# Kernel optimization log

Hardware: AMD Instinct MI355X
Metric: run time of the kernel (lower is better)

The kernel has to match this reference:

```python
import jax, jax.numpy as jnp
import numpy as np

B, N, I = 8, 1024, 64
E, H, D = 2, 2, 128   # edge types, heads per layer, hidden dim
O = 64                # num_outputs
IN1 = E * H * D       # layer-1 filter input dim (concat of layer-0 heads)


def setup_inputs() -> dict:
    key = jax.random.key(0)
    ks = jax.random.split(key, 20)
    s = lambda f: 1.0 / np.sqrt(f)
    inp = {
        "nodes": jax.random.normal(ks[0], (B, N, I), jnp.float32),
        "edges": jax.random.normal(ks[1], (B, N, N, E), jnp.float32) * 0.1,
        "Wemb": jax.random.normal(ks[2], (I, D), jnp.float32) * s(I),
        "bemb": jnp.zeros((D,), jnp.float32),
        # layer 0 params: filter W, att nets a1/a2 (weight + bias), state bias
        "W0":   jax.random.normal(ks[3], (E, H, D, D), jnp.float32) * s(D),
        "A1w0": jax.random.normal(ks[4], (E, H, D), jnp.float32) * s(D),
        "A1b0": jnp.zeros((E, H), jnp.float32),
        "A2w0": jax.random.normal(ks[5], (E, H, D), jnp.float32) * s(D),
        "A2b0": jnp.zeros((E, H), jnp.float32),
        "SB0":  jnp.zeros((E, H, D), jnp.float32),
        # layer 1 params (input dim = E*H*D from concat)
        "W1":   jax.random.normal(ks[6], (E, H, IN1, D), jnp.float32) * s(IN1),
        "A1w1": jax.random.normal(ks[7], (E, H, D), jnp.float32) * s(D),
        "A1b1": jnp.zeros((E, H), jnp.float32),
        "A2w1": jax.random.normal(ks[8], (E, H, D), jnp.float32) * s(D),
        "A2b1": jnp.zeros((E, H), jnp.float32),
        "SB1":  jnp.zeros((E, H, D), jnp.float32),
        "Wout": jax.random.normal(ks[9], (D, O), jnp.float32) * s(D),
        "bout": jnp.zeros((O,), jnp.float32),
    }
    return inp


def _gat_layer(state, edges_ebnn, W, a1w, a1b, a2w, a2b, sb):
    # state: (B,N,Fin); W: (E,H,Fin,D); edges_ebnn: (E,1,B,N,N)
    Wh = jnp.einsum('bni,ehid->ehbnd', state, W)                    # (E,H,B,N,D)
    s1 = jnp.einsum('ehbnd,ehd->ehbn', Wh, a1w) + a1b[:, :, None, None]
    s2 = jnp.einsum('ehbnd,ehd->ehbn', Wh, a2w) + a2b[:, :, None, None]
    att = s1[..., :, None] + s2[..., None, :]                       # a1_i + a2_j
    att = jax.nn.leaky_relu(att, 0.2) + edges_ebnn                  # edge-type bias
    att = jax.nn.softmax(att, axis=-2)                              # torch dim=1 (over i)
    msg = jnp.einsum('ehbij,ehbjd->ehbid', att, Wh)                 # bmm aggregation
    return msg + sb[:, :, None, None, :]                            # (E,H,B,N,D)


def reference(nodes, edges, Wemb, bemb,
              W0, A1w0, A1b0, A2w0, A2b0, SB0,
              W1, A1w1, A1b1, A2w1, A2b1, SB1,
              Wout, bout):
    edges_e = jnp.transpose(edges, (3, 0, 1, 2))[:, None]           # (E,1,B,N,N)
    state = jax.nn.relu(nodes @ Wemb + bemb)                        # SlimFC embedding
    # layer 0: concat heads/edgetypes along feature dim (torch order jj outer, ii inner)
    m0 = _gat_layer(state, edges_e, W0, A1w0, A1b0, A2w0, A2b0, SB0)
    state = jnp.transpose(m0, (2, 3, 0, 1, 4)).reshape(B, N, E * H * D)
    # layer 1 (last): elu then mean over all heads/edgetypes
    m1 = jax.nn.elu(_gat_layer(state, edges_e, W1, A1w1, A1b1, A2w1, A2b1, SB1))
    state = jnp.mean(m1, axis=(0, 1))                               # (B,N,D)
    return state @ Wout + bout                                      # (B,N,O)
```

## Files before the change

kernel.cpp:

```cpp
#include <hip/hip_runtime.h>
#include <hip/hip_bf16.h>
#include <math.h>

#define NB 8
#define NN 1024
#define NI 64
#define EHC 4
#define ND 128
#define NO 64
#define FIN1 512
#define BN 8192

typedef __attribute__((ext_vector_type(8))) short short8;
typedef __attribute__((ext_vector_type(4))) float f32x4;

__device__ __forceinline__ unsigned short f2bf(float f) {
    union { float f; unsigned u; } v; v.f = f;
    unsigned r = v.u + 0x7FFF + ((v.u >> 16) & 1);
    return (unsigned short)(r >> 16);
}

__global__ void prepTk(const float* __restrict__ W0, const float* __restrict__ W1,
                       const float* __restrict__ Wemb, unsigned short* __restrict__ W0T,
                       unsigned short* __restrict__ W1T, unsigned short* __restrict__ WembT) {
    int idx = blockIdx.x * 256 + threadIdx.x;
    if (idx < EHC * ND * ND) {
        int eh = idx >> 14, d = (idx >> 7) & 127, k = idx & 127;
        W0T[idx] = f2bf(W0[((size_t)(eh * ND + k)) * ND + d]);
    }
    int idx1 = idx - EHC * ND * ND;
    if (idx1 >= 0 && idx1 < EHC * ND * FIN1) {
        int eh = idx1 >> 16;
        int r = idx1 & 65535;
        int d = r >> 9, k = r & 511;
        W1T[idx1] = f2bf(W1[((size_t)(eh * FIN1 + k)) * ND + d]);
    }
    int idx2 = idx - (EHC * ND * ND + EHC * ND * FIN1);
    if (idx2 >= 0 && idx2 < ND * NI) {
        int d = idx2 >> 6, k = idx2 & 63;
        WembT[idx2] = f2bf(Wemb[k * ND + d]);
    }
}

__global__ __launch_bounds__(256, 4) void embwh0k(
    const float* __restrict__ nodes, const unsigned short* __restrict__ WembT,
    const float* __restrict__ bemb, const unsigned short* __restrict__ W0T,
    unsigned short* __restrict__ WhT, const float* __restrict__ a1w,
    const float* __restrict__ a1b, const float* __restrict__ a2w,
    const float* __restrict__ a2b, float* __restrict__ s1, float* __restrict__ s2) {
    int id = blockIdx.x;
    int g = id & 7, s_ = id >> 3;
    int eh = s_ & 3;
    int row0 = ((s_ >> 2) * 8 + g) * 32;
    int t = threadIdx.x;
    int w = t >> 6, lane = t & 63;
    int m = lane & 15, quad = lane >> 4;

    __shared__ unsigned short stateL[32 * 136];

    f32x4 accE[2][2];
#pragma unroll
    for (int mt = 0; mt < 2; ++mt)
#pragma unroll
        for (int nt = 0; nt < 2; ++nt) accE[mt][nt] = (f32x4){0.f, 0.f, 0.f, 0.f};
#pragma unroll
    for (int kt = 0; kt < 2; ++kt) {
        short8 aE[2], bE[2];
#pragma unroll
        for (int mt = 0; mt < 2; ++mt) {
            const float* np = nodes + (size_t)(row0 + mt * 16 + m) * NI + kt * 32 + quad * 8;
            f32x4 v0 = *(const f32x4*)np;
            f32x4 v1 = *(const f32x4*)(np + 4);
            union { unsigned short us[8]; short8 s8; } pk;
#pragma unroll
            for (int r = 0; r < 4; ++r) {
                pk.us[r] = f2bf(v0[r]);
                pk.us[r + 4] = f2bf(v1[r]);
            }
            aE[mt] = pk.s8;
        }
#pragma unroll
        for (int nt = 0; nt < 2; ++nt)
            bE[nt] = *(const short8*)(WembT + (w * 32 + nt * 16 + m) * NI + kt * 32 + quad * 8);
#pragma unroll
        for (int mt = 0; mt < 2; ++mt)
#pragma unroll
            for (int nt = 0; nt < 2; ++nt)
                accE[mt][nt] =
                    __builtin_amdgcn_mfma_f32_16x16x32_bf16(aE[mt], bE[nt], accE[mt][nt], 0, 0, 0);
    }
#pragma unroll
    for (int mt = 0; mt < 2; ++mt)
#pragma unroll
        for (int nt = 0; nt < 2; ++nt) {
            int d = w * 32 + nt * 16 + m;
            float bb = bemb[d];
#pragma unroll
            for (int r = 0; r < 4; ++r) {
                float v = fmaxf(accE[mt][nt][r] + bb, 0.f);
                stateL[(mt * 16 + quad * 4 + r) * 136 + d] = f2bf(v);
            }
        }
    __syncthreads();

    f32x4 acc[2][2];
#pragma unroll
    for (int mt = 0; mt < 2; ++mt)
#pragma unroll
        for (int nt = 0; nt < 2; ++nt) acc[mt][nt] = (f32x4){0.f, 0.f, 0.f, 0.f};
#pragma unroll
    for (int k0 = 0; k0 < ND; k0 += 32) {
        short8 a[2], b[2];
#pragma unroll
        for (int mt = 0; mt < 2; ++mt)
            a[mt] = *(const short8*)&stateL[(mt * 16 + m) * 136 + k0 + quad * 8];
#pragma unroll
        for (int nt = 0; nt < 2; ++nt)
            b[nt] = *(const short8*)(W0T + ((size_t)(eh * ND + w * 32 + nt * 16 + m)) * ND +
                                     k0 + quad * 8);
#pragma unroll
        for (int mt = 0; mt < 2; ++mt)
#pragma unroll
            for (int nt = 0; nt < 2; ++nt)
                acc[mt][nt] =
                    __builtin_amdgcn_mfma_f32_16x16x32_bf16(a[mt], b[nt], acc[mt][nt], 0, 0, 0);
    }

    int b_ = row0 >> 10, i0b = row0 & 1023;
    int ehb = eh * NB + b_;
#pragma unroll
    for (int mt = 0; mt < 2; ++mt)
#pragma unroll
        for (int nt = 0; nt < 2; ++nt) {
            int d = w * 32 + nt * 16 + m;
            int i = i0b + mt * 16 + quad * 4;
            union { unsigned short us[4]; unsigned long long u64; } pk;
#pragma unroll
            for (int r = 0; r < 4; ++r) pk.us[r] = f2bf(acc[mt][nt][r]);
            *(unsigned long long*)(WhT + (((size_t)ehb) * ND + d) * NN + i) = pk.u64;
        }
    float w1a = a1w[eh * ND + w * 32 + m], w1b = a1w[eh * ND + w * 32 + 16 + m];
    float w2a = a2w[eh * ND + w * 32 + m], w2b = a2w[eh * ND + w * 32 + 16 + m];
    float p1[2][4], p2[2][4];
#pragma unroll
    for (int mt = 0; mt < 2; ++mt)
#pragma unroll
        for (int r = 0; r < 4; ++r) {
            p1[mt][r] = acc[mt][0][r] * w1a + acc[mt][1][r] * w1b;
            p2[mt][r] = acc[mt][0][r] * w2a + acc[mt][1][r] * w2b;
        }
#pragma unroll
    for (int off = 8; off >= 1; off >>= 1)
#pragma unroll
        for (int mt = 0; mt < 2; ++mt)
#pragma unroll
            for (int r = 0; r < 4; ++r) {
                p1[mt][r] += __shfl_xor(p1[mt][r], off);
                p2[mt][r] += __shfl_xor(p2[mt][r], off);
            }
    __shared__ float sred[2][4][4][8];
    if (m == 0) {
#pragma unroll
        for (int mt = 0; mt < 2; ++mt)
#pragma unroll
            for (int r = 0; r < 4; ++r) {
                sred[0][w][quad][mt * 4 + r] = p1[mt][r];
                sred[1][w][quad][mt * 4 + r] = p2[mt][r];
            }
    }
    __syncthreads();
    if (t < 32) {
        int mt = t >> 4, quad2 = (t >> 2) & 3, r = t & 3;
        int c = mt * 4 + r;
        float v = sred[0][0][quad2][c] + sred[0][1][quad2][c] + sred[0][2][quad2][c] +
                  sred[0][3][quad2][c];
        s1[(size_t)ehb * NN + i0b + t] = v + a1b[eh];
    } else if (t < 64) {
        int tl = t - 32;
        int mt = tl >> 4, quad2 = (tl >> 2) & 3, r = tl & 3;
        int c = mt * 4 + r;
        float v = sred[1][0][quad2][c] + sred[1][1][quad2][c] + sred[1][2][quad2][c] +
                  sred[1][3][quad2][c];
        s2[(size_t)ehb * NN + i0b + tl] = v + a2b[eh];
    }
}

__global__ __launch_bounds__(256, 4) void whgemm1k(
    const unsigned short* __restrict__ state, const unsigned short* __restrict__ WT,
    unsigned short* __restrict__ WhT, const float* __restrict__ a1w,
    const float* __restrict__ a1b, const float* __restrict__ a2w,
    const float* __restrict__ a2b, float* __restrict__ s1, float* __restrict__ s2) {
    int id = blockIdx.x;
    int g = id & 7, s_ = id >> 3;
    int eh = s_ & 3;
    int row0 = ((s_ >> 2) * 8 + g) * 32;
    int t = threadIdx.x;
    int w = t >> 6, lane = t & 63;
    int m = lane & 15, quad = lane >> 4;

    f32x4 acc[2][2];
#pragma unroll
    for (int mt = 0; mt < 2; ++mt)
#pragma unroll
        for (int nt = 0; nt < 2; ++nt) acc[mt][nt] = (f32x4){0.f, 0.f, 0.f, 0.f};

    const unsigned short* Ab = state + (size_t)(row0 + m) * FIN1 + quad * 8;
    const unsigned short* Bb = WT + ((size_t)eh * ND + w * 32 + m) * FIN1 + quad * 8;
#pragma unroll 4
    for (int k0 = 0; k0 < FIN1; k0 += 32) {
        short8 a[2], b[2];
#pragma unroll
        for (int mt = 0; mt < 2; ++mt)
            a[mt] = *(const short8*)(Ab + (size_t)mt * 16 * FIN1 + k0);
#pragma unroll
        for (int nt = 0; nt < 2; ++nt)
            b[nt] = *(const short8*)(Bb + (size_t)nt * 16 * FIN1 + k0);
#pragma unroll
        for (int mt = 0; mt < 2; ++mt)
#pragma unroll
            for (int nt = 0; nt < 2; ++nt)
                acc[mt][nt] =
                    __builtin_amdgcn_mfma_f32_16x16x32_bf16(a[mt], b[nt], acc[mt][nt], 0, 0, 0);
    }
    int b_ = row0 >> 10, i0b = row0 & 1023;
    int ehb = eh * NB + b_;
#pragma unroll
    for (int mt = 0; mt < 2; ++mt)
#pragma unroll
        for (int nt = 0; nt < 2; ++nt) {
            int d = w * 32 + nt * 16 + m;
            int i = i0b + mt * 16 + quad * 4;
            union { unsigned short us[4]; unsigned long long u64; } pk;
#pragma unroll
            for (int r = 0; r < 4; ++r) pk.us[r] = f2bf(acc[mt][nt][r]);
            *(unsigned long long*)(WhT + (((size_t)ehb) * ND + d) * NN + i) = pk.u64;
        }
    float w1a = a1w[eh * ND + w * 32 + m], w1b = a1w[eh * ND + w * 32 + 16 + m];
    float w2a = a2w[eh * ND + w * 32 + m], w2b = a2w[eh * ND + w * 32 + 16 + m];
    float p1[2][4], p2[2][4];
#pragma unroll
    for (int mt = 0; mt < 2; ++mt)
#pragma unroll
        for (int r = 0; r < 4; ++r) {
            p1[mt][r] = acc[mt][0][r] * w1a + acc[mt][1][r] * w1b;
            p2[mt][r] = acc[mt][0][r] * w2a + acc[mt][1][r] * w2b;
        }
#pragma unroll
    for (int off = 8; off >= 1; off >>= 1)
#pragma unroll
        for (int mt = 0; mt < 2; ++mt)
#pragma unroll
            for (int r = 0; r < 4; ++r) {
                p1[mt][r] += __shfl_xor(p1[mt][r], off);
                p2[mt][r] += __shfl_xor(p2[mt][r], off);
            }
    __shared__ float sred[2][4][4][8];
    if (m == 0) {
#pragma unroll
        for (int mt = 0; mt < 2; ++mt)
#pragma unroll
            for (int r = 0; r < 4; ++r) {
                sred[0][w][quad][mt * 4 + r] = p1[mt][r];
                sred[1][w][quad][mt * 4 + r] = p2[mt][r];
            }
    }
    __syncthreads();
    if (t < 32) {
        int mt = t >> 4, quad2 = (t >> 2) & 3, r = t & 3;
        int c = mt * 4 + r;
        float v = sred[0][0][quad2][c] + sred[0][1][quad2][c] + sred[0][2][quad2][c] +
                  sred[0][3][quad2][c];
        s1[(size_t)ehb * NN + i0b + t] = v + a1b[eh];
    } else if (t < 64) {
        int tl = t - 32;
        int mt = tl >> 4, quad2 = (tl >> 2) & 3, r = tl & 3;
        int c = mt * 4 + r;
        float v = sred[1][0][quad2][c] + sred[1][1][quad2][c] + sred[1][2][quad2][c] +
                  sred[1][3][quad2][c];
        s2[(size_t)ehb * NN + i0b + tl] = v + a2b[eh];
    }
}

__global__ __launch_bounds__(256, 4) void colsumk(const float* __restrict__ edges,
                                                  const float* __restrict__ s1,
                                                  const float* __restrict__ s2,
                                                  float* __restrict__ Spart) {
    int jt = blockIdx.x, b = blockIdx.y, ic = blockIdx.z;
    int t = threadIdx.x;
    int jp = t & 31, is = t >> 5;
    int j = jt * 64 + jp * 2;
    __shared__ float s1L[4][128];
    for (int idx = t; idx < 512; idx += 256) {
        int eh = idx >> 7;
        s1L[eh][idx & 127] = s1[((size_t)eh * NB + b) * NN + ic * 128 + (idx & 127)];
    }
    __syncthreads();
    float s2v[4][2], acc4[4][2];
#pragma unroll
    for (int eh = 0; eh < 4; ++eh) {
        s2v[eh][0] = s2[((size_t)eh * NB + b) * NN + j];
        s2v[eh][1] = s2[((size_t)eh * NB + b) * NN + j + 1];
        acc4[eh][0] = 0.f;
        acc4[eh][1] = 0.f;
    }
    const float4* ep = (const float4*)edges +
                       (size_t)(b * NN + ic * 128 + is * 16) * (NN / 2) + jt * 32 + jp;
#pragma unroll 4
    for (int ii = 0; ii < 16; ++ii) {
        float4 ev = ep[(size_t)ii * (NN / 2)];
        float s1v = s1L[0][is * 16 + ii];
#pragma unroll
        for (int eh = 0; eh < 4; ++eh) {
            float sv = s1L[eh][is * 16 + ii];
            float x0 = sv + s2v[eh][0];
            x0 = fmaxf(x0, 0.2f * x0);
            acc4[eh][0] += __expf(x0 + (eh < 2 ? ev.x : ev.y));
            float x1 = sv + s2v[eh][1];
            x1 = fmaxf(x1, 0.2f * x1);
            acc4[eh][1] += __expf(x1 + (eh < 2 ? ev.z : ev.w));
        }
        (void)s1v;
    }
    __shared__ float red[8][4][64];
#pragma unroll
    for (int eh = 0; eh < 4; ++eh) {
        red[is][eh][jp * 2] = acc4[eh][0];
        red[is][eh][jp * 2 + 1] = acc4[eh][1];
    }
    __syncthreads();
    if (t < 256) {
        int eho = t >> 6, jlo = t & 63;
        float Sv = 0.f;
#pragma unroll
        for (int isx = 0; isx < 8; ++isx) Sv += red[isx][eho][jlo];
        Spart[(((size_t)ic * EHC + eho) * NB + b) * NN + jt * 64 + jlo] = Sv;
    }
}

__global__ __launch_bounds__(512, 4) void msgk(const float* __restrict__ edges,
                                               const unsigned short* __restrict__ WhT,
                                               const float* __restrict__ s1,
                                               const float* __restrict__ s2,
                                               const float* __restrict__ Spart,
                                               const float* __restrict__ sb,
                                               unsigned short* __restrict__ out0,
                                               float* __restrict__ out1, int mode) {
    int id = blockIdx.x;
    int b = id & 7;
    int s_ = id >> 3;
    int eh = s_ & 3;
    int itile = s_ >> 2;
    int e = eh >> 1;
    int i0 = itile * 64;
    int t = threadIdx.x;
    int w = t >> 6, lane = t & 63;
    int n = lane & 15, quad = lane >> 4;
    int jl = t & 63, ib = w;

    __shared__ float2 stL[NN];
    __shared__ unsigned short pA[2][64 * 72];

    int base = (eh * NB + b) * NN;
    const size_t pstr = (size_t)EHC * NB * NN;
    for (int jj = t; jj < NN; jj += 512) {
        float S = 0.f;
#pragma unroll
        for (int ic = 0; ic < 8; ++ic) S += Spart[(size_t)ic * pstr + base + jj];
        stL[jj] = make_float2(s2[base + jj], __logf(S));
    }
    float s1r[8];
    {
        const f32x4* sp = (const f32x4*)(s1 + base + i0 + ib * 8);
        f32x4 v0 = sp[0], v1 = sp[1];
#pragma unroll
        for (int r = 0; r < 4; ++r) { s1r[r] = v0[r]; s1r[r + 4] = v1[r]; }
    }

    f32x4 acc[4];
#pragma unroll
    for (int nt = 0; nt < 4; ++nt) acc[nt] = (f32x4){0.f, 0.f, 0.f, 0.f};

    const unsigned short* Ab =
        WhT + ((size_t)base * ND + (size_t)(w * 16 + n) * NN) + quad * 8;
    const float2* ep = (const float2*)edges + (size_t)(b * NN + i0 + ib * 8) * NN + jl;
    __syncthreads();

    float2 evA[8], evB[8];
    short8 aA[2], aB[2];

    auto loadE = [&](float2* ev, int j0) {
#pragma unroll
        for (int q = 0; q < 8; ++q) ev[q] = ep[(size_t)q * NN + j0];
    };
    auto loadA = [&](short8* av, int j0) {
#pragma unroll
        for (int kt = 0; kt < 2; ++kt)
            av[kt] = *(const short8*)(Ab + kt * 32 + j0);
    };
    auto pstep = [&](const float2* ev, const short8* av, int j0, int buf) {
        float2 stj = stL[j0 + jl];
#pragma unroll
        for (int q = 0; q < 8; ++q) {
            float edge = e ? ev[q].y : ev[q].x;
            float x = s1r[q] + stj.x;
            x = fmaxf(x, 0.2f * x);
            pA[buf][(ib * 8 + q) * 72 + jl] = f2bf(__expf(x + edge - stj.y));
        }
        __syncthreads();
#pragma unroll
        for (int kt = 0; kt < 2; ++kt) {
            short8 bv[4];
#pragma unroll
            for (int nt = 0; nt < 4; ++nt)
                bv[nt] = *(const short8*)&pA[buf][(nt * 16 + n) * 72 + kt * 32 + quad * 8];
#pragma unroll
            for (int nt = 0; nt < 4; ++nt)
                acc[nt] =
                    __builtin_amdgcn_mfma_f32_16x16x32_bf16(av[kt], bv[nt], acc[nt], 0, 0, 0);
        }
    };

    loadE(evA, 0);
    loadA(aA, 0);
    for (int sp2 = 0; sp2 < 8; ++sp2) {
        int j0 = sp2 * 128;
        loadE(evB, j0 + 64);
        loadA(aB, j0 + 64);
        pstep(evA, aA, j0, 0);
        if (sp2 < 7) {
            loadE(evA, j0 + 128);
            loadA(aA, j0 + 128);
        }
        pstep(evB, aB, j0 + 64, 1);
    }

    {
        int d0 = w * 16 + quad * 4;
        f32x4 sbv = *(const f32x4*)&sb[eh * ND + d0];
#pragma unroll
        for (int nt = 0; nt < 4; ++nt) {
            int i = i0 + nt * 16 + n;
            if (mode == 0) {
                union { unsigned short us[4]; unsigned long long u64; } pk;
#pragma unroll
                for (int r = 0; r < 4; ++r) pk.us[r] = f2bf(acc[nt][r] + sbv[r]);
                *(unsigned long long*)(out0 + (size_t)(b * NN + i) * FIN1 + eh * ND + d0) =
                    pk.u64;
            } else {
                f32x4 vv;
#pragma unroll
                for (int r = 0; r < 4; ++r) {
                    float v = acc[nt][r] + sbv[r];
                    vv[r] = v > 0.f ? v : expm1f(v);
                }
                *(f32x4*)(out1 + ((size_t)(eh * NB + b) * NN + i) * ND + d0) = vv;
            }
        }
    }
}

__global__ __launch_bounds__(256) void finalk(const float* __restrict__ m1,
                                              const float* __restrict__ Wout,
                                              const float* __restrict__ bout,
                                              float* __restrict__ out) {
    int row0 = blockIdx.x * 16;
    int t = threadIdx.x;
    __shared__ float sF[16 * ND];
    __shared__ float wL[ND * NO];
    const size_t str = (size_t)BN * ND;
    for (int idx = t; idx < 16 * ND; idx += 256) {
        size_t r = (size_t)row0 * ND + idx;
        sF[idx] = 0.25f * (m1[r] + m1[r + str] + m1[r + 2 * str] + m1[r + 3 * str]);
    }
    for (int idx = t; idx < ND * NO; idx += 256) wL[idx] = Wout[idx];
    __syncthreads();
    int o = t & 63;
    int rr = t >> 6;
    float bo = bout[o];
#pragma unroll
    for (int q = 0; q < 4; ++q) {
        int r = rr * 4 + q;
        float acc = 0.f;
#pragma unroll 4
        for (int d = 0; d < ND; ++d) acc += sF[r * ND + d] * wL[d * NO + o];
        out[(size_t)(row0 + r) * NO + o] = acc + bo;
    }
}

extern "C" void kernel_launch(void* const* d_in, const int* in_sizes, int n_in,
                              void* d_out, int out_size, void* d_ws, size_t ws_size,
                              hipStream_t stream) {
    const float* nodes = (const float*)d_in[0];
    const float* edges = (const float*)d_in[1];
    const float* Wemb = (const float*)d_in[2];
    const float* bemb = (const float*)d_in[3];
    const float* W0 = (const float*)d_in[4];
    const float* A1w0 = (const float*)d_in[5];
    const float* A1b0 = (const float*)d_in[6];
    const float* A2w0 = (const float*)d_in[7];
    const float* A2b0 = (const float*)d_in[8];
    const float* SB0 = (const float*)d_in[9];
    const float* W1 = (const float*)d_in[10];
    const float* A1w1 = (const float*)d_in[11];
    const float* A1b1 = (const float*)d_in[12];
    const float* A2w1 = (const float*)d_in[13];
    const float* A2b1 = (const float*)d_in[14];
    const float* SB1 = (const float*)d_in[15];
    const float* Wout = (const float*)d_in[16];
    const float* bout = (const float*)d_in[17];
    float* out = (float*)d_out;

    char* p = (char*)d_ws;
    auto alloc = [&](size_t bytes) {
        char* r = p;
        p += (bytes + 255) & ~(size_t)255;
        return r;
    };
    unsigned short* W0T = (unsigned short*)alloc((size_t)EHC * ND * ND * 2);
    unsigned short* W1T = (unsigned short*)alloc((size_t)EHC * ND * FIN1 * 2);
    unsigned short* WembT = (unsigned short*)alloc((size_t)ND * NI * 2);
    unsigned short* WhT = (unsigned short*)alloc((size_t)EHC * BN * ND * 2);
    unsigned short* state1 = (unsigned short*)alloc((size_t)BN * FIN1 * 2);
    float* s1b = (float*)alloc((size_t)EHC * BN * 4);
    float* s2b = (float*)alloc((size_t)EHC * BN * 4);
    float* Spart = (float*)alloc((size_t)8 * EHC * BN * 4);
    float* m1 = (float*)alloc((size_t)EHC * BN * ND * 4);

    prepTk<<<1312, 256, 0, stream>>>(W0, W1, Wemb, W0T, W1T, WembT);
    embwh0k<<<1024, 256, 0, stream>>>(nodes, WembT, bemb, W0T, WhT, A1w0, A1b0, A2w0, A2b0,
                                      s1b, s2b);
    colsumk<<<dim3(NN / 64, NB, 8), 256, 0, stream>>>(edges, s1b, s2b, Spart);
    msgk<<<512, 512, 0, stream>>>(edges, WhT, s1b, s2b, Spart, SB0, state1, m1, 0);
    whgemm1k<<<1024, 256, 0, stream>>>(state1, W1T, WhT, A1w1, A1b1, A2w1, A2b1, s1b, s2b);
    colsumk<<<dim3(NN / 64, NB, 8), 256, 0, stream>>>(edges, s1b, s2b, Spart);
    msgk<<<512, 512, 0, stream>>>(edges, WhT, s1b, s2b, Spart, SB1, state1, m1, 1);
    finalk<<<BN / 16, 256, 0, stream>>>(m1, Wout, bout, out);
}
```

Measured before the change: 274.2 us.

## Materialize bf16 attention probabilities and fold softmax normalization into Wh

The column-sum kernel now also writes the unnormalized exp attention scores for every head to a large bf16 buffer. The softmax is over i, so its per-column 1/S_j factor is applied to Wh in a new small kernel (whnk), which is stored in fp32 beforehand. The message kernel then becomes a plain bf16 MFMA GEMM over the stored probabilities instead of recomputing exp from edges and staging through shared memory. This removes the duplicated exp work and the LDS round trip, but adds a 64 MB write and read of probabilities per layer, plus extra fp32 Wh traffic.

```diff
diff --git a/kernel.cpp b/kernel.cpp
--- a/kernel.cpp
+++ b/kernel.cpp
@@ -13,11 +13,17 @@
 
 typedef __attribute__((ext_vector_type(8))) short short8;
 typedef __attribute__((ext_vector_type(4))) float f32x4;
+typedef __attribute__((ext_vector_type(4))) unsigned int u32x4;
 
 __device__ __forceinline__ unsigned short f2bf(float f) {
     union { float f; unsigned u; } v; v.f = f;
     unsigned r = v.u + 0x7FFF + ((v.u >> 16) & 1);
     return (unsigned short)(r >> 16);
+}
+__device__ __forceinline__ unsigned pack2bf(float f0, float f1) {
+    union { float f; unsigned u; } a, b;
+    a.f = f0; b.f = f1;
+    return __builtin_amdgcn_perm(b.u + 0x8000u, a.u + 0x8000u, 0x07060302u);
 }
 
 __global__ void prepTk(const float* __restrict__ W0, const float* __restrict__ W1,
@@ -45,7 +51,7 @@
 __global__ __launch_bounds__(256, 4) void embwh0k(
     const float* __restrict__ nodes, const unsigned short* __restrict__ WembT,
     const float* __restrict__ bemb, const unsigned short* __restrict__ W0T,
-    unsigned short* __restrict__ WhT, const float* __restrict__ a1w,
+    float* __restrict__ Whf, const float* __restrict__ a1w,
     const float* __restrict__ a1b, const float* __restrict__ a2w,
     const float* __restrict__ a2b, float* __restrict__ s1, float* __restrict__ s2) {
     int id = blockIdx.x;
@@ -71,11 +77,11 @@
             const float* np = nodes + (size_t)(row0 + mt * 16 + m) * NI + kt * 32 + quad * 8;
             f32x4 v0 = *(const f32x4*)np;
             f32x4 v1 = *(const f32x4*)(np + 4);
-            union { unsigned short us[8]; short8 s8; } pk;
-#pragma unroll
-            for (int r = 0; r < 4; ++r) {
-                pk.us[r] = f2bf(v0[r]);
-                pk.us[r + 4] = f2bf(v1[r]);
+            union { unsigned us[4]; short8 s8; } pk;
+#pragma unroll
+            for (int r = 0; r < 2; ++r) {
+                pk.us[r] = pack2bf(v0[2 * r], v0[2 * r + 1]);
+                pk.us[r + 2] = pack2bf(v1[2 * r], v1[2 * r + 1]);
             }
             aE[mt] = pk.s8;
         }
@@ -134,10 +140,7 @@
         for (int nt = 0; nt < 2; ++nt) {
             int d = w * 32 + nt * 16 + m;
             int i = i0b + mt * 16 + quad * 4;
-            union { unsigned short us[4]; unsigned long long u64; } pk;
-#pragma unroll
-            for (int r = 0; r < 4; ++r) pk.us[r] = f2bf(acc[mt][nt][r]);
-            *(unsigned long long*)(WhT + (((size_t)ehb) * ND + d) * NN + i) = pk.u64;
+            *(f32x4*)(Whf + (((size_t)ehb) * ND + d) * NN + i) = acc[mt][nt];
         }
     float w1a = a1w[eh * ND + w * 32 + m], w1b = a1w[eh * ND + w * 32 + 16 + m];
     float w2a = a2w[eh * ND + w * 32 + m], w2b = a2w[eh * ND + w * 32 + 16 + m];
@@ -187,7 +190,7 @@
 
 __global__ __launch_bounds__(256, 4) void whgemm1k(
     const unsigned short* __restrict__ state, const unsigned short* __restrict__ WT,
-    unsigned short* __restrict__ WhT, const float* __restrict__ a1w,
+    float* __restrict__ Whf, const float* __restrict__ a1w,
     const float* __restrict__ a1b, const float* __restrict__ a2w,
     const float* __restrict__ a2b, float* __restrict__ s1, float* __restrict__ s2) {
     int id = blockIdx.x;
@@ -230,10 +233,7 @@
         for (int nt = 0; nt < 2; ++nt) {
             int d = w * 32 + nt * 16 + m;
             int i = i0b + mt * 16 + quad * 4;
-            union { unsigned short us[4]; unsigned long long u64; } pk;
-#pragma unroll
-            for (int r = 0; r < 4; ++r) pk.us[r] = f2bf(acc[mt][nt][r]);
-            *(unsigned long long*)(WhT + (((size_t)ehb) * ND + d) * NN + i) = pk.u64;
+            *(f32x4*)(Whf + (((size_t)ehb) * ND + d) * NN + i) = acc[mt][nt];
         }
     float w1a = a1w[eh * ND + w * 32 + m], w1b = a1w[eh * ND + w * 32 + 16 + m];
     float w2a = a2w[eh * ND + w * 32 + m], w2b = a2w[eh * ND + w * 32 + 16 + m];
@@ -284,7 +284,8 @@
 __global__ __launch_bounds__(256, 4) void colsumk(const float* __restrict__ edges,
                                                   const float* __restrict__ s1,
                                                   const float* __restrict__ s2,
-                                                  float* __restrict__ Spart) {
+                                                  float* __restrict__ Spart,
+                                                  unsigned* __restrict__ Pbuf) {
     int jt = blockIdx.x, b = blockIdx.y, ic = blockIdx.z;
     int t = threadIdx.x;
     int jp = t & 31, is = t >> 5;
@@ -305,21 +306,24 @@
     }
     const float4* ep = (const float4*)edges +
                        (size_t)(b * NN + ic * 128 + is * 16) * (NN / 2) + jt * 32 + jp;
-#pragma unroll 4
+#pragma unroll 2
     for (int ii = 0; ii < 16; ++ii) {
         float4 ev = ep[(size_t)ii * (NN / 2)];
-        float s1v = s1L[0][is * 16 + ii];
+        int i = ic * 128 + is * 16 + ii;
 #pragma unroll
         for (int eh = 0; eh < 4; ++eh) {
             float sv = s1L[eh][is * 16 + ii];
             float x0 = sv + s2v[eh][0];
             x0 = fmaxf(x0, 0.2f * x0);
-            acc4[eh][0] += __expf(x0 + (eh < 2 ? ev.x : ev.y));
+            float p0 = __expf(x0 + (eh < 2 ? ev.x : ev.y));
             float x1 = sv + s2v[eh][1];
             x1 = fmaxf(x1, 0.2f * x1);
-            acc4[eh][1] += __expf(x1 + (eh < 2 ? ev.z : ev.w));
-        }
-        (void)s1v;
+            float p1v = __expf(x1 + (eh < 2 ? ev.z : ev.w));
+            acc4[eh][0] += p0;
+            acc4[eh][1] += p1v;
+            Pbuf[((size_t)(eh * NB + b) * NN + i) * (NN / 2) + jt * 32 + jp] =
+                pack2bf(p0, p1v);
+        }
     }
     __shared__ float red[8][4][64];
 #pragma unroll
@@ -337,123 +341,101 @@
     }
 }
 
-__global__ __launch_bounds__(512, 4) void msgk(const float* __restrict__ edges,
-                                               const unsigned short* __restrict__ WhT,
-                                               const float* __restrict__ s1,
-                                               const float* __restrict__ s2,
-                                               const float* __restrict__ Spart,
+__global__ __launch_bounds__(256) void whnk(const float* __restrict__ Whf,
+                                            const float* __restrict__ Spart,
+                                            unsigned short* __restrict__ Whn) {
+    int blk = blockIdx.x;
+    int ehb = blk & 31, jc = blk >> 5;
+    int t = threadIdx.x;
+    __shared__ float rS[128];
+    if (t < 128) {
+        int j = jc * 128 + t;
+        const size_t pstr = (size_t)EHC * NB * NN;
+        float S = 0.f;
+#pragma unroll
+        for (int ic = 0; ic < 8; ++ic) S += Spart[(size_t)ic * pstr + (size_t)ehb * NN + j];
+        rS[t] = 1.f / S;
+    }
+    __syncthreads();
+#pragma unroll
+    for (int it = 0; it < 8; ++it) {
+        int idx = it * 256 + t;
+        int d = idx >> 4, jq = idx & 15;
+        int j = jc * 128 + jq * 8;
+        const float* wp = Whf + ((size_t)ehb * ND + d) * NN + j;
+        f32x4 v0 = *(const f32x4*)wp;
+        f32x4 v1 = *(const f32x4*)(wp + 4);
+        u32x4 o;
+        o[0] = pack2bf(v0[0] * rS[jq * 8 + 0], v0[1] * rS[jq * 8 + 1]);
+        o[1] = pack2bf(v0[2] * rS[jq * 8 + 2], v0[3] * rS[jq * 8 + 3]);
+        o[2] = pack2bf(v1[0] * rS[jq * 8 + 4], v1[1] * rS[jq * 8 + 5]);
+        o[3] = pack2bf(v1[2] * rS[jq * 8 + 6], v1[3] * rS[jq * 8 + 7]);
+        *(u32x4*)(Whn + ((size_t)ehb * ND + d) * NN + j) = o;
+    }
+}
+
+__global__ __launch_bounds__(256, 4) void msgk(const unsigned short* __restrict__ Whn,
+                                               const unsigned short* __restrict__ Pbuf,
                                                const float* __restrict__ sb,
                                                unsigned short* __restrict__ out0,
                                                float* __restrict__ out1, int mode) {
     int id = blockIdx.x;
-    int b = id & 7;
-    int s_ = id >> 3;
-    int eh = s_ & 3;
-    int itile = s_ >> 2;
-    int e = eh >> 1;
-    int i0 = itile * 64;
+    int ehb = id & 31;
+    int it = id >> 5;
+    int eh = ehb >> 3, b = ehb & 7;
+    int i0 = it * 32;
     int t = threadIdx.x;
     int w = t >> 6, lane = t & 63;
-    int n = lane & 15, quad = lane >> 4;
-    int jl = t & 63, ib = w;
-
-    __shared__ float2 stL[NN];
-    __shared__ unsigned short pA[2][64 * 72];
-
-    int base = (eh * NB + b) * NN;
-    const size_t pstr = (size_t)EHC * NB * NN;
-    for (int jj = t; jj < NN; jj += 512) {
-        float S = 0.f;
-#pragma unroll
-        for (int ic = 0; ic < 8; ++ic) S += Spart[(size_t)ic * pstr + base + jj];
-        stL[jj] = make_float2(s2[base + jj], __logf(S));
-    }
-    float s1r[8];
-    {
-        const f32x4* sp = (const f32x4*)(s1 + base + i0 + ib * 8);
-        f32x4 v0 = sp[0], v1 = sp[1];
-#pragma unroll
-        for (int r = 0; r < 4; ++r) { s1r[r] = v0[r]; s1r[r + 4] = v1[r]; }
-    }
-
-    f32x4 acc[4];
-#pragma unroll
-    for (int nt = 0; nt < 4; ++nt) acc[nt] = (f32x4){0.f, 0.f, 0.f, 0.f};
-
-    const unsigned short* Ab =
-        WhT + ((size_t)base * ND + (size_t)(w * 16 + n) * NN) + quad * 8;
-    const float2* ep = (const float2*)edges + (size_t)(b * NN + i0 + ib * 8) * NN + jl;
-    __syncthreads();
-
-    float2 evA[8], evB[8];
-    short8 aA[2], aB[2];
-
-    auto loadE = [&](float2* ev, int j0) {
-#pragma unroll
-        for (int q = 0; q < 8; ++q) ev[q] = ep[(size_t)q * NN + j0];
-    };
-    auto loadA = [&](short8* av, int j0) {
-#pragma unroll
-        for (int kt = 0; kt < 2; ++kt)
-            av[kt] = *(const short8*)(Ab + kt * 32 + j0);
-    };
-    auto pstep = [&](const float2* ev, const short8* av, int j0, int buf) {
-        float2 stj = stL[j0 + jl];
-#pragma unroll
-        for (int q = 0; q < 8; ++q) {
-            float edge = e ? ev[q].y : ev[q].x;
-            float x = s1r[q] + stj.x;
-            x = fmaxf(x, 0.2f * x);
-            pA[buf][(ib * 8 + q) * 72 + jl] = f2bf(__expf(x + edge - stj.y));
-        }
-        __syncthreads();
-#pragma unroll
-        for (int kt = 0; kt < 2; ++kt) {
-            short8 bv[4];
-#pragma unroll
-            for (int nt = 0; nt < 4; ++nt)
-                bv[nt] = *(const short8*)&pA[buf][(nt * 16 + n) * 72 + kt * 32 + quad * 8];
-#pragma unroll
-            for (int nt = 0; nt < 4; ++nt)
-                acc[nt] =
-                    __builtin_amdgcn_mfma_f32_16x16x32_bf16(av[kt], bv[nt], acc[nt], 0, 0, 0);
-        }
-    };
-
-    loadE(evA, 0);
-    loadA(aA, 0);
-    for (int sp2 = 0; sp2 < 8; ++sp2) {
-        int j0 = sp2 * 128;
-        loadE(evB, j0 + 64);
-        loadA(aB, j0 + 64);
-        pstep(evA, aA, j0, 0);
-        if (sp2 < 7) {
-            loadE(evA, j0 + 128);
-            loadA(aA, j0 + 128);
-        }
-        pstep(evB, aB, j0 + 64, 1);
-    }
-
-    {
-        int d0 = w * 16 + quad * 4;
+    int m = lane & 15, quad = lane >> 4;
+
+    f32x4 acc[2][2];
+#pragma unroll
+    for (int mt = 0; mt < 2; ++mt)
+#pragma unroll
+        for (int nt = 0; nt < 2; ++nt) acc[mt][nt] = (f32x4){0.f, 0.f, 0.f, 0.f};
+
+    const unsigned short* Ab = Whn + ((size_t)ehb * ND + w * 32 + m) * NN + quad * 8;
+    const unsigned short* Bb = Pbuf ? (const unsigned short*)0 : (const unsigned short*)0;
+    const unsigned short* Pb = Pbuf + ((size_t)ehb * NN + i0 + m) * NN + quad * 8;
+    (void)Bb;
+#pragma unroll 4
+    for (int k0 = 0; k0 < NN; k0 += 32) {
+        short8 a[2], bv[2];
+#pragma unroll
+        for (int mt = 0; mt < 2; ++mt)
+            a[mt] = *(const short8*)(Ab + (size_t)mt * 16 * NN + k0);
+#pragma unroll
+        for (int nt = 0; nt < 2; ++nt)
+            bv[nt] = *(const short8*)(Pb + (size_t)nt * 16 * NN + k0);
+#pragma unroll
+        for (int mt = 0; mt < 2; ++mt)
+#pragma unroll
+            for (int nt = 0; nt < 2; ++nt)
+                acc[mt][nt] =
+                    __builtin_amdgcn_mfma_f32_16x16x32_bf16(a[mt], bv[nt], acc[mt][nt], 0, 0, 0);
+    }
+
+#pragma unroll
+    for (int mt = 0; mt < 2; ++mt) {
+        int d0 = w * 32 + mt * 16 + quad * 4;
         f32x4 sbv = *(const f32x4*)&sb[eh * ND + d0];
 #pragma unroll
-        for (int nt = 0; nt < 4; ++nt) {
-            int i = i0 + nt * 16 + n;
+        for (int nt = 0; nt < 2; ++nt) {
+            int i = i0 + nt * 16 + m;
             if (mode == 0) {
-                union { unsigned short us[4]; unsigned long long u64; } pk;
-#pragma unroll
-                for (int r = 0; r < 4; ++r) pk.us[r] = f2bf(acc[nt][r] + sbv[r]);
+                union { unsigned us[2]; unsigned long long u64; } pk;
+                pk.us[0] = pack2bf(acc[mt][nt][0] + sbv[0], acc[mt][nt][1] + sbv[1]);
+                pk.us[1] = pack2bf(acc[mt][nt][2] + sbv[2], acc[mt][nt][3] + sbv[3]);
                 *(unsigned long long*)(out0 + (size_t)(b * NN + i) * FIN1 + eh * ND + d0) =
                     pk.u64;
             } else {
                 f32x4 vv;
 #pragma unroll
                 for (int r = 0; r < 4; ++r) {
-                    float v = acc[nt][r] + sbv[r];
+                    float v = acc[mt][nt][r] + sbv[r];
                     vv[r] = v > 0.f ? v : expm1f(v);
                 }
-                *(f32x4*)(out1 + ((size_t)(eh * NB + b) * NN + i) * ND + d0) = vv;
+                *(f32x4*)(out1 + ((size_t)ehb * NN + i) * ND + d0) = vv;
             }
         }
     }
@@ -519,7 +501,9 @@
     unsigned short* W0T = (unsigned short*)alloc((size_t)EHC * ND * ND * 2);
     unsigned short* W1T = (unsigned short*)alloc((size_t)EHC * ND * FIN1 * 2);
     unsigned short* WembT = (unsigned short*)alloc((size_t)ND * NI * 2);
-    unsigned short* WhT = (unsigned short*)alloc((size_t)EHC * BN * ND * 2);
+    float* Whf = (float*)alloc((size_t)EHC * BN * ND * 4);
+    unsigned short* Whn = (unsigned short*)alloc((size_t)EHC * BN * ND * 2);
+    unsigned* Pbuf = (unsigned*)alloc((size_t)EHC * NB * NN * (NN / 2) * 4);
     unsigned short* state1 = (unsigned short*)alloc((size_t)BN * FIN1 * 2);
     float* s1b = (float*)alloc((size_t)EHC * BN * 4);
     float* s2b = (float*)alloc((size_t)EHC * BN * 4);
@@ -527,12 +511,14 @@
     float* m1 = (float*)alloc((size_t)EHC * BN * ND * 4);
 
     prepTk<<<1312, 256, 0, stream>>>(W0, W1, Wemb, W0T, W1T, WembT);
-    embwh0k<<<1024, 256, 0, stream>>>(nodes, WembT, bemb, W0T, WhT, A1w0, A1b0, A2w0, A2b0,
+    embwh0k<<<1024, 256, 0, stream>>>(nodes, WembT, bemb, W0T, Whf, A1w0, A1b0, A2w0, A2b0,
                                       s1b, s2b);
-    colsumk<<<dim3(NN / 64, NB, 8), 256, 0, stream>>>(edges, s1b, s2b, Spart);
-    msgk<<<512, 512, 0, stream>>>(edges, WhT, s1b, s2b, Spart, SB0, state1, m1, 0);
-    whgemm1k<<<1024, 256, 0, stream>>>(state1, W1T, WhT, A1w1, A1b1, A2w1, A2b1, s1b, s2b);
-    colsumk<<<dim3(NN / 64, NB, 8), 256, 0, stream>>>(edges, s1b, s2b, Spart);
-    msgk<<<512, 512, 0, stream>>>(edges, WhT, s1b, s2b, Spart, SB1, state1, m1, 1);
+    colsumk<<<dim3(NN / 64, NB, 8), 256, 0, stream>>>(edges, s1b, s2b, Spart, Pbuf);
+    whnk<<<256, 256, 0, stream>>>(Whf, Spart, Whn);
+    msgk<<<1024, 256, 0, stream>>>(Whn, (const unsigned short*)Pbuf, SB0, state1, m1, 0);
+    whgemm1k<<<1024, 256, 0, stream>>>(state1, W1T, Whf, A1w1, A1b1, A2w1, A2b1, s1b, s2b);
+    colsumk<<<dim3(NN / 64, NB, 8), 256, 0, stream>>>(edges, s1b, s2b, Spart, Pbuf);
+    whnk<<<256, 256, 0, stream>>>(Whf, Spart, Whn);
+    msgk<<<1024, 256, 0, stream>>>(Whn, (const unsigned short*)Pbuf, SB1, state1, m1, 1);
     finalk<<<BN / 16, 256, 0, stream>>>(m1, Wout, bout, out);
 }
```

Result: slower. 361.3 us (+31.8%).
